# Kernel optimization log

Measured on AMD Instinct MI355X. Metric: run time of the kernel, lower is better.

The kernel has to match this reference:

```python
import jax, jax.numpy as jnp
import numpy as np

NUE, NAP, E = 512, 1024, 524288
D, OC, HID, PH = 4, 64, 32, 4  # raw feat dim, out_channels, out//2, power hid


def _lin(key, fi, fo):
    k1, k2 = jax.random.split(key)
    s = 1.0 / np.sqrt(fi)
    W = jax.random.uniform(k1, (fi, fo), minval=-s, maxval=s, dtype=jnp.float32)
    b = jax.random.uniform(k2, (fo,), minval=-s, maxval=s, dtype=jnp.float32)
    return W, b


_LAYER_SPECS = [
    ("c1_msg", D + D, HID), ("c1_upd", HID + D, OC - D), ("c1_ew", 3 * D, OC - D),
    ("c2_msg", OC + D, HID), ("c2_upd", HID + D, OC - D), ("c2_ew", D + OC + D, OC - D),
    ("c3u_msg", 2 * OC, HID), ("c3u_upd", HID + OC, OC - D), ("c3u_ew", 3 * OC, OC - D),
    ("c3d_msg", 2 * OC, HID), ("c3d_upd", HID + OC, OC - D), ("c3d_ew", 3 * OC, OC - D),
    ("pe1", OC, PH), ("pe2", PH, 1),
]


def setup_inputs() -> dict:
    key = jax.random.key(0)
    ks = jax.random.split(key, 24)
    inp = {}
    inp["x_ue"] = jax.random.normal(ks[0], (NUE, D), dtype=jnp.float32)
    inp["x_ap"] = jax.random.normal(ks[1], (NAP, D), dtype=jnp.float32)
    inp["ea_up"] = jax.random.normal(ks[2], (E, D), dtype=jnp.float32)
    inp["ea_down"] = jax.random.normal(ks[3], (E, D), dtype=jnp.float32)
    inp["ei_up_src"] = jax.random.randint(ks[4], (E,), 0, NUE, dtype=jnp.int32)
    inp["ei_up_dst"] = jax.random.randint(ks[5], (E,), 0, NAP, dtype=jnp.int32)
    inp["ei_down_src"] = jax.random.randint(ks[6], (E,), 0, NAP, dtype=jnp.int32)
    inp["ei_down_dst"] = jax.random.randint(ks[7], (E,), 0, NUE, dtype=jnp.int32)
    for i, (n, fi, fo) in enumerate(_LAYER_SPECS):
        W, b = _lin(ks[8 + i], fi, fo)
        inp[n + "_W"] = W
        inp[n + "_b"] = b
    inp["pe_ln_g"] = jnp.ones((PH,), dtype=jnp.float32)
    inp["pe_ln_b"] = jnp.zeros((PH,), dtype=jnp.float32)
    return inp


def _lrelu(x):
    return jnp.where(x >= 0, x, 0.1 * x)


def _mlp1(x, W, b):  # one MLP block: Linear -> LeakyReLU(0.1) (dropout = eval identity)
    return _lrelu(x @ W + b)


def _conv_step(x_src, x_dst, ea, src_idx, dst_idx, n_dst,
               msg_W, msg_b, upd_W, upd_b, ew_W, ew_b, residual):
    xj = x_src[src_idx]                                   # [E, d_src] gather
    m = _mlp1(jnp.concatenate([xj, ea], axis=1), msg_W, msg_b)  # [E, HID]
    agg = jax.ops.segment_sum(m, dst_idx, num_segments=n_dst)   # scatter-add -> [n_dst, HID]
    tmp = _mlp1(jnp.concatenate([x_dst, agg], axis=1), upd_W, upd_b)  # [n_dst, OC-D]
    if residual:
        tmp = tmp + x_dst[:, D:]
    new_x_dst = jnp.concatenate([x_dst[:, :D], tmp], axis=1)     # [n_dst, OC]
    xi = x_dst[dst_idx]                                   # old x_dst per torch code
    e = _mlp1(jnp.concatenate([xj, ea, xi], axis=1), ew_W, ew_b)  # [E, OC-D]
    new_ea = jnp.concatenate([ea[:, :D], e], axis=1)             # [E, OC]
    return new_x_dst, new_ea


def _layernorm(x, g, b, eps=1e-5):
    mu = jnp.mean(x, axis=-1, keepdims=True)
    var = jnp.mean(jnp.square(x - mu), axis=-1, keepdims=True)
    return (x - mu) * jax.lax.rsqrt(var + eps) * g + b


def reference(x_ue, x_ap, ea_up, ea_down,
              ei_up_src, ei_up_dst, ei_down_src, ei_down_dst,
              c1_msg_W, c1_msg_b, c1_upd_W, c1_upd_b, c1_ew_W, c1_ew_b,
              c2_msg_W, c2_msg_b, c2_upd_W, c2_upd_b, c2_ew_W, c2_ew_b,
              c3u_msg_W, c3u_msg_b, c3u_upd_W, c3u_upd_b, c3u_ew_W, c3u_ew_b,
              c3d_msg_W, c3d_msg_b, c3d_upd_W, c3d_upd_b, c3d_ew_W, c3d_ew_b,
              pe1_W, pe1_b, pe2_W, pe2_b, pe_ln_g, pe_ln_b):
    # conv1: UE --up--> AP
    x_ap, ea_up = _conv_step(x_ue, x_ap, ea_up, ei_up_src, ei_up_dst, NAP,
                             c1_msg_W, c1_msg_b, c1_upd_W, c1_upd_b, c1_ew_W, c1_ew_b, False)
    # conv2: AP --down--> UE
    x_ue, ea_down = _conv_step(x_ap, x_ue, ea_down, ei_down_src, ei_down_dst, NUE,
                               c2_msg_W, c2_msg_b, c2_upd_W, c2_upd_b, c2_ew_W, c2_ew_b, False)
    # conv3 handles both edge types (residual since src_dim == out_channels)
    x_ap, ea_up = _conv_step(x_ue, x_ap, ea_up, ei_up_src, ei_up_dst, NAP,
                             c3u_msg_W, c3u_msg_b, c3u_upd_W, c3u_upd_b, c3u_ew_W, c3u_ew_b, True)
    x_ue, ea_down = _conv_step(x_ap, x_ue, ea_down, ei_down_src, ei_down_dst, NUE,
                               c3d_msg_W, c3d_msg_b, c3d_upd_W, c3d_upd_b, c3d_ew_W, c3d_ew_b, True)
    # power head on down edges: Lin -> LayerNorm -> LeakyReLU -> Lin
    h = _lrelu(_layernorm(ea_down @ pe1_W + pe1_b, pe_ln_g, pe_ln_b))
    power = h @ pe2_W + pe2_b                                   # [E, 1]
    ea_down = jnp.concatenate([ea_down[:, :D], power], axis=1)  # [E, D+1]
    return (x_ue, x_ap, ea_up, ea_down)
```

## Files before the change

### kernel.cpp

```cpp
#include <hip/hip_runtime.h>

typedef __attribute__((ext_vector_type(8))) short bf16x8;
typedef __attribute__((ext_vector_type(4))) float f32x4;

static constexpr int EN   = 524288;
static constexpr int NUE_ = 512;
static constexpr int NAP_ = 1024;
static constexpr int HID_ = 32;
static constexpr int OD_  = 60;
static constexpr int OC_  = 64;
static constexpr int NB_  = 256;
static constexpr int CH_  = EN / NB_;

__device__ __forceinline__ unsigned short f2bf(float x) {
  unsigned int u = __float_as_uint(x);
  return (unsigned short)((u + 0x7fffu + ((u >> 16) & 1u)) >> 16);
}
__device__ __forceinline__ float bf2f(unsigned int u) {
  return __uint_as_float(u << 16);
}

__global__ __launch_bounds__(256)
void lhist2x(const int* __restrict__ up_dst, const int* __restrict__ dn_dst,
             int* __restrict__ bh_up, int* __restrict__ bh_dn,
             unsigned short* __restrict__ lr_up, unsigned short* __restrict__ lr_dn,
             const float* __restrict__ c3u_ew, const float* __restrict__ c3u_msg,
             const float* __restrict__ c3d_ew, const float* __restrict__ c3d_msg,
             unsigned short* __restrict__ we3u, unsigned short* __restrict__ wm3u,
             unsigned short* __restrict__ we3d, unsigned short* __restrict__ wm3d,
             const float* __restrict__ x_ue, const float* __restrict__ x_ap,
             const float* __restrict__ c1_ew, const float* __restrict__ c1_msg,
             const float* __restrict__ c1_ew_b, const float* __restrict__ c1_msg_b,
             const float* __restrict__ c2_ew, const float* __restrict__ c2_ew_b,
             float* __restrict__ Y1j, float* __restrict__ Y1i,
             float* __restrict__ Y1m, float* __restrict__ Y2i)
{
  __shared__ int h[NAP_];
  const int t = threadIdx.x;
  if (blockIdx.x >= 2 * NB_) {
    const int xb = blockIdx.x - 2 * NB_;
    if (xb < 48) {
      const float* W; unsigned short* out; int NREAL, NPAD, i;
      if (xb < 16)      { W = c3u_ew;  out = we3u; NREAL = 60; NPAD = 64; i = xb * 256 + t; }
      else if (xb < 24) { W = c3u_msg; out = wm3u; NREAL = 32; NPAD = 32; i = (xb - 16) * 256 + t; }
      else if (xb < 40) { W = c3d_ew;  out = we3d; NREAL = 60; NPAD = 64; i = (xb - 24) * 256 + t; }
      else              { W = c3d_msg; out = wm3d; NREAL = 32; NPAD = 32; i = (xb - 40) * 256 + t; }
      if (i >= NPAD * 64) return;
      int n = i >> 6, k = i & 63;
      float v = (n < NREAL) ? W[(size_t)(64 + k) * NREAL + n] : 0.f;
      out[i] = f2bf(v);
    } else {
      const int tid = (xb - 48) * 256 + t;
      if (tid < NUE_) {
        const float4 x = *reinterpret_cast<const float4*>(x_ue + (size_t)tid * 4);
        const float xv[4] = {x.x, x.y, x.z, x.w};
        for (int o = 0; o < OD_; ++o) {
          float a = 0.f, bb = c2_ew_b[o];
          #pragma unroll
          for (int k = 0; k < 4; ++k) {
            a = fmaf(xv[k], c1_ew[k * OD_ + o], a);
            bb = fmaf(xv[k], c2_ew[(68 + k) * OD_ + o], bb);
          }
          Y1j[(size_t)tid * OD_ + o] = a;
          Y2i[(size_t)tid * OD_ + o] = bb;
        }
        for (int o = 0; o < HID_; ++o) {
          float m = c1_msg_b[o];
          #pragma unroll
          for (int k = 0; k < 4; ++k) m = fmaf(xv[k], c1_msg[k * HID_ + o], m);
          Y1m[(size_t)tid * HID_ + o] = m;
        }
      } else if (tid < NUE_ + NAP_) {
        const int r = tid - NUE_;
        const float4 x = *reinterpret_cast<const float4*>(x_ap + (size_t)r * 4);
        const float xv[4] = {x.x, x.y, x.z, x.w};
        for (int o = 0; o < OD_; ++o) {
          float a = c1_ew_b[o];
          #pragma unroll
          for (int k = 0; k < 4; ++k) a = fmaf(xv[k], c1_ew[(8 + k) * OD_ + o], a);
          Y1i[(size_t)r * OD_ + o] = a;
        }
      }
    }
    return;
  }
  const bool up = blockIdx.x < NB_;
  const int b = up ? blockIdx.x : blockIdx.x - NB_;
  const int NBINS = up ? NAP_ : NUE_;
  const int* dst = up ? up_dst : dn_dst;
  int* bh = up ? bh_up : bh_dn;
  unsigned short* lrank = up ? lr_up : lr_dn;
  for (int i = t; i < NBINS; i += 256) h[i] = 0;
  __syncthreads();
  const int base = b * CH_;
  #pragma unroll 1
  for (int i = t; i < CH_; i += 256)
    lrank[base + i] = (unsigned short)atomicAdd(&h[dst[base + i]], 1);
  __syncthreads();
  for (int i = t; i < NBINS; i += 256)
    bh[(size_t)i * NB_ + b] = h[i];
}

__global__ __launch_bounds__(64)
void bscanA2(int* __restrict__ bh_up, int* __restrict__ bh_dn,
             int* __restrict__ bs_up, int* __restrict__ bs_dn)
{
  const bool up = blockIdx.x < NAP_;
  const int bin = up ? blockIdx.x : blockIdx.x - NAP_;
  int* bh = up ? bh_up : bh_dn;
  int* binsum = up ? bs_up : bs_dn;
  const int l = threadIdx.x;
  int4 v = *reinterpret_cast<int4*>(&bh[(size_t)bin * NB_ + l * 4]);
  const int s0 = v.x, s1 = s0 + v.y, s2 = s1 + v.z, s3 = s2 + v.w;
  int inc = s3;
  #pragma unroll
  for (int d2 = 1; d2 < 64; d2 <<= 1) {
    int n = __shfl_up(inc, d2, 64);
    if (l >= d2) inc += n;
  }
  const int exc = inc - s3;
  int4 o; o.x = exc; o.y = exc + s0; o.z = exc + s1; o.w = exc + s2;
  *reinterpret_cast<int4*>(&bh[(size_t)bin * NB_ + l * 4]) = o;
  if (l == 63) binsum[bin] = inc;
}

__global__ __launch_bounds__(256)
void bscanB2(const int* __restrict__ bs_up, int* __restrict__ off_up,
             const int* __restrict__ bs_dn, int* __restrict__ off_dn)
{
  const bool up = blockIdx.x == 0;
  const int NBINS = up ? NAP_ : NUE_;
  const int K = NBINS / 256;
  const int* binsum = up ? bs_up : bs_dn;
  int* off = up ? off_up : off_dn;
  __shared__ int wtot[4];
  const int t = threadIdx.x, lane = t & 63, wid = t >> 6;
  int loc[4]; int s = 0;
  for (int k = 0; k < K; ++k) { loc[k] = binsum[t * K + k]; s += loc[k]; }
  int inc = s;
  #pragma unroll
  for (int d2 = 1; d2 < 64; d2 <<= 1) {
    int n = __shfl_up(inc, d2, 64);
    if (lane >= d2) inc += n;
  }
  if (lane == 63) wtot[wid] = inc;
  __syncthreads();
  int woff = 0;
  #pragma unroll
  for (int ww = 0; ww < 4; ++ww) if (ww < wid) woff += wtot[ww];
  int a = woff + inc - s;
  for (int k = 0; k < K; ++k) { off[t * K + k] = a; a += loc[k]; }
  if (t == 255) off[NBINS] = a;
}

__global__ __launch_bounds__(256)
void rankc2(const int* __restrict__ up_dst, const int* __restrict__ up_src,
            const int* __restrict__ dn_dst, const int* __restrict__ dn_src,
            const unsigned short* __restrict__ lr_up, const unsigned short* __restrict__ lr_dn,
            const int* __restrict__ bh_up, const int* __restrict__ bh_dn,
            const int* __restrict__ off_up, const int* __restrict__ off_dn,
            int* __restrict__ rank_dn,
            int* __restrict__ perm_up, int* __restrict__ srcP_up, int* __restrict__ dstP_up,
            int* __restrict__ perm_dn, int* __restrict__ srcP_dn, int* __restrict__ dstP_dn)
{
  const int gid = blockIdx.x * 256 + threadIdx.x;
  const bool up = gid < EN;
  const int e = up ? gid : gid - EN;
  const int* dst = up ? up_dst : dn_dst;
  const int* src = up ? up_src : dn_src;
  const unsigned short* lrank = up ? lr_up : lr_dn;
  const int* bh = up ? bh_up : bh_dn;
  const int* off = up ? off_up : off_dn;
  const int blk = e / CH_;
  const int d = dst[e];
  const int rk = off[d] + bh[(size_t)d * NB_ + blk] + (int)lrank[e];
  if (up) {
    perm_up[rk] = e; srcP_up[rk] = src[e]; dstP_up[rk] = d;
  } else {
    rank_dn[e] = rk;
    perm_dn[rk] = e; srcP_dn[rk] = src[e]; dstP_dn[rk] = d;
  }
}

__global__ __launch_bounds__(256)
void e12n(const float* __restrict__ ea_in,
          const int* __restrict__ perm, const int* __restrict__ srcP,
          const int* __restrict__ off,
          const float* __restrict__ Yje, const float* __restrict__ Yie,
          const float* __restrict__ Ym,
          const float* __restrict__ We,
          const float* __restrict__ Wm,
          unsigned short* __restrict__ outB,
          const float* __restrict__ x_in,
          const float* __restrict__ W, const float* __restrict__ b,
          float* __restrict__ x_out,
          const float* __restrict__ WtA, float* __restrict__ YA,
          const float* __restrict__ WtB, const float* __restrict__ bB, float* __restrict__ YB,
          const float* __restrict__ WtC, const float* __restrict__ bC, float* __restrict__ YC)
{
  __shared__ unsigned short Eb[64 * 72];
  __shared__ float RedF[64][33];
  __shared__ float Part[8][33];
  __shared__ float Ag[32];
  __shared__ float Xr[4];
  __shared__ float Xn[OC_];
  const int d = blockIdx.x, t = threadIdx.x;
  const int beg = off[d], end = off[d + 1];
  const int r = t >> 2, j = t & 3;
  const int c0 = j * 15, m0 = j * 8;
  if (t < 4) Xr[t] = x_in[(size_t)d * 4 + t];
  float yie[15];
  #pragma unroll
  for (int c = 0; c < 15; ++c) yie[c] = Yie[(size_t)d * OD_ + c0 + c];
  float am[8] = {0.f, 0.f, 0.f, 0.f, 0.f, 0.f, 0.f, 0.f};

  for (int sb = beg; sb < end; sb += 64) {
    const int slot = sb + r;
    const bool act = slot < end;
    const int e = act ? perm[slot] : 0;
    const int s = act ? srcP[slot] : 0;
    float4 ea = act ? *reinterpret_cast<const float4*>(ea_in + (size_t)e * 4)
                    : make_float4(0.f, 0.f, 0.f, 0.f);
    const float eav[4] = {ea.x, ea.y, ea.z, ea.w};
    float acc[15];
    #pragma unroll
    for (int c = 0; c < 15; ++c) acc[c] = Yje[(size_t)s * OD_ + c0 + c] + yie[c];
    #pragma unroll
    for (int k = 0; k < 4; ++k)
      #pragma unroll
      for (int c = 0; c < 15; ++c)
        acc[c] = fmaf(eav[k], We[k * OD_ + c0 + c], acc[c]);
    if (act) {
      #pragma unroll
      for (int c = 0; c < 15; ++c) {
        float v = acc[c] >= 0.f ? acc[c] : 0.1f * acc[c];
        Eb[r * 72 + 4 + c0 + c] = f2bf(v);
      }
      if (j == 0) {
        Eb[r * 72 + 0] = f2bf(ea.x); Eb[r * 72 + 1] = f2bf(ea.y);
        Eb[r * 72 + 2] = f2bf(ea.z); Eb[r * 72 + 3] = f2bf(ea.w);
      }
    }
    float m[8];
    #pragma unroll
    for (int c = 0; c < 8; ++c) m[c] = Ym[(size_t)s * HID_ + m0 + c];
    #pragma unroll
    for (int k = 0; k < 4; ++k)
      #pragma unroll
      for (int c = 0; c < 8; ++c)
        m[c] = fmaf(eav[k], Wm[k * HID_ + m0 + c], m[c]);
    if (act) {
      #pragma unroll
      for (int c = 0; c < 8; ++c)
        am[c] += m[c] >= 0.f ? m[c] : 0.1f * m[c];
    }
    __syncthreads();
    const int nact = end - sb < 64 ? end - sb : 64;
    for (int idx = t; idx < nact * 8; idx += 256) {
      int row = idx >> 3, ch = idx & 7;
      *reinterpret_cast<uint4*>(outB + (size_t)(sb + row) * OC_ + ch * 8) =
          *reinterpret_cast<const uint4*>(&Eb[row * 72 + ch * 8]);
    }
    __syncthreads();
  }
  #pragma unroll
  for (int c = 0; c < 8; ++c) RedF[r][m0 + c] = am[c];
  __syncthreads();
  {
    const int col = t & 31, g = t >> 5;
    float s = 0.f;
    #pragma unroll
    for (int r2 = 0; r2 < 8; ++r2) s += RedF[g * 8 + r2][col];
    Part[g][col] = s;
  }
  __syncthreads();
  if (t < 32) {
    float s = 0.f;
    #pragma unroll
    for (int g2 = 0; g2 < 8; ++g2) s += Part[g2][t];
    Ag[t] = s;
  }
  __syncthreads();
  if (t < OD_) {
    float acc = b[t];
    #pragma unroll
    for (int k = 0; k < 4; ++k) acc = fmaf(Xr[k], W[k * OD_ + t], acc);
    #pragma unroll 4
    for (int k = 0; k < HID_; ++k) acc = fmaf(Ag[k], W[(4 + k) * OD_ + t], acc);
    acc = acc >= 0.f ? acc : 0.1f * acc;
    x_out[(size_t)d * OC_ + 4 + t] = acc;
    Xn[4 + t] = acc;
  } else if (t < OC_) {
    x_out[(size_t)d * OC_ + (t - OD_)] = Xr[t - OD_];
    Xn[t - OD_] = Xr[t - OD_];
  }
  __syncthreads();
  if (t < OD_) {
    float a = 0.f;
    #pragma unroll 4
    for (int k = 0; k < OC_; ++k) a = fmaf(Xn[k], WtA[k * OD_ + t], a);
    YA[(size_t)d * OD_ + t] = a;
  } else if (t >= 64 && t < 96) {
    const int cc = t - 64;
    float a = bB[cc];
    #pragma unroll 4
    for (int k = 0; k < OC_; ++k) a = fmaf(Xn[k], WtB[k * HID_ + cc], a);
    YB[(size_t)d * HID_ + cc] = a;
  } else if (t >= 128 && t < 188) {
    const int cc = t - 128;
    float a = bC[cc];
    #pragma unroll 4
    for (int k = 0; k < OC_; ++k) a = fmaf(Xn[k], WtC[k * OD_ + cc], a);
    YC[(size_t)d * OD_ + cc] = a;
  }
}

template<bool FUSE>
__global__ __launch_bounds__(256)
void edge3(const unsigned short* __restrict__ eaB,
           const float* __restrict__ ea0_src,
           const int* __restrict__ perm,
           const int* __restrict__ srcP, const int* __restrict__ dstP,
           const unsigned short* __restrict__ Wet, const unsigned short* __restrict__ Wmt,
           const float* __restrict__ Yje, const float* __restrict__ Yie,
           const float* __restrict__ Ym,
           unsigned int* __restrict__ msg32,
           float* __restrict__ ea_out,
           float* __restrict__ pT,
           const float* __restrict__ pe1_W)
{
  const int t = threadIdx.x, l = t & 63, w = t >> 6;
  const int lr = l & 15, lkb = l >> 4;
  const int sW = blockIdx.x * 256 + w * 64;

  bf16x8 be[4][2], bm[2][2];
  #pragma unroll
  for (int nt = 0; nt < 4; ++nt)
    #pragma unroll
    for (int kk = 0; kk < 2; ++kk)
      be[nt][kk] = *reinterpret_cast<const bf16x8*>(Wet + (nt * 16 + lr) * 64 + kk * 32 + lkb * 8);
  #pragma unroll
  for (int nt = 0; nt < 2; ++nt)
    #pragma unroll
    for (int kk = 0; kk < 2; ++kk)
      bm[nt][kk] = *reinterpret_cast<const bf16x8*>(Wmt + (nt * 16 + lr) * 64 + kk * 32 + lkb * 8);

  #pragma unroll 1
  for (int tile = 0; tile < 4; ++tile) {
    const int s0t = sW + tile * 16;
    const unsigned short* ar = eaB + (size_t)(s0t + lr) * OC_ + lkb * 8;
    bf16x8 a[2];
    a[0] = *reinterpret_cast<const bf16x8*>(ar);
    a[1] = *reinterpret_cast<const bf16x8*>(ar + 32);

    f32x4 accE[4] = {f32x4{0,0,0,0}, f32x4{0,0,0,0}, f32x4{0,0,0,0}, f32x4{0,0,0,0}};
    f32x4 accM[2] = {f32x4{0,0,0,0}, f32x4{0,0,0,0}};
    #pragma unroll
    for (int kk = 0; kk < 2; ++kk) {
      #pragma unroll
      for (int nt = 0; nt < 4; ++nt)
        accE[nt] = __builtin_amdgcn_mfma_f32_16x16x32_bf16(a[kk], be[nt][kk], accE[nt], 0, 0, 0);
      #pragma unroll
      for (int nt = 0; nt < 2; ++nt)
        accM[nt] = __builtin_amdgcn_mfma_f32_16x16x32_bf16(a[kk], bm[nt][kk], accM[nt], 0, 0, 0);
    }
    #pragma unroll
    for (int r = 0; r < 4; ++r) {
      const int sl = s0t + lkb * 4 + r;
      const int s = srcP[sl], d = dstP[sl];
      float v0 = accM[0][r] + Ym[(size_t)s * HID_ + lr];
      float v1 = accM[1][r] + Ym[(size_t)s * HID_ + 16 + lr];
      v0 = v0 >= 0.f ? v0 : 0.1f * v0;
      v1 = v1 >= 0.f ? v1 : 0.1f * v1;
      const int q0 = (2 * lr) & 15, q1 = (2 * lr + 1) & 15;
      float t00 = __shfl(v0, q0, 16), t10 = __shfl(v1, q0, 16);
      float t01 = __shfl(v0, q1, 16), t11 = __shfl(v1, q1, 16);
      float lo = (lr < 8) ? t00 : t10;
      float hi = (lr < 8) ? t01 : t11;
      msg32[(size_t)sl * 16 + lr] = ((unsigned)f2bf(hi) << 16) | f2bf(lo);

      float val[4];
      #pragma unroll
      for (int nt = 0; nt < 4; ++nt) {
        int col = nt * 16 + lr;
        float v = (col < OD_)
            ? accE[nt][r] + Yje[(size_t)s * OD_ + col] + Yie[(size_t)d * OD_ + col]
            : 0.f;
        val[nt] = v >= 0.f ? v : 0.1f * v;
      }
      if constexpr (!FUSE) {
        const int e = perm[sl];
        #pragma unroll
        for (int nt = 0; nt < 4; ++nt) {
          int col = nt * 16 + lr;
          if (col < OD_) ea_out[(size_t)e * OC_ + 4 + col] = val[nt];
        }
        if (lr == 0) {
          float4 ea0 = *reinterpret_cast<const float4*>(ea0_src + (size_t)e * 4);
          *reinterpret_cast<float4*>(ea_out + (size_t)e * OC_) = ea0;
        }
      } else {
        float p4[4] = {0.f, 0.f, 0.f, 0.f};
        #pragma unroll
        for (int nt = 0; nt < 4; ++nt) {
          int col = nt * 16 + lr;
          if (col < OD_) {
            #pragma unroll
            for (int jj = 0; jj < 4; ++jj)
              p4[jj] = fmaf(val[nt], pe1_W[(4 + col) * 4 + jj], p4[jj]);
          }
        }
        #pragma unroll
        for (int mk = 1; mk < 16; mk <<= 1) {
          #pragma unroll
          for (int jj = 0; jj < 4; ++jj)
            p4[jj] += __shfl_xor(p4[jj], mk, 64);
        }
        if (lr == 0)
          *reinterpret_cast<float4*>(pT + (size_t)sl * 4) =
              make_float4(p4[0], p4[1], p4[2], p4[3]);
      }
    }
  }
}

template<int LX, bool RES>
__device__ __forceinline__
void nodeup_body(int d, int t,
                 const float* __restrict__ x_in,
                 const unsigned int* __restrict__ msg32,
                 const int* __restrict__ off,
                 const float* __restrict__ W, const float* __restrict__ b,
                 float* __restrict__ x_out,
                 const float* WtA, float* YA,
                 const float* WtB, const float* bB, float* YB)
{
  __shared__ float Pb[16][32];
  __shared__ float Ag[32];
  __shared__ float Xr[LX];
  __shared__ float Xn[OC_];
  const int beg = off[d], end = off[d + 1];
  const int c = t & 15, g = t >> 4;
  float px = 0.f, py = 0.f;
  for (int i = beg + g; i < end; i += 16) {
    unsigned u = msg32[(size_t)i * 16 + c];
    px += bf2f(u & 0xffffu);
    py += bf2f(u >> 16);
  }
  Pb[g][2 * c] = px; Pb[g][2 * c + 1] = py;
  if (t < LX) Xr[t] = x_in[(size_t)d * LX + t];
  __syncthreads();
  if (t < 32) {
    float s = 0.f;
    #pragma unroll
    for (int g2 = 0; g2 < 16; ++g2) s += Pb[g2][t];
    Ag[t] = s;
  }
  __syncthreads();
  if (t < OD_) {
    float acc = b[t];
    #pragma unroll 4
    for (int k = 0; k < LX; ++k) acc = fmaf(Xr[k], W[k * OD_ + t], acc);
    #pragma unroll 4
    for (int k = 0; k < HID_; ++k) acc = fmaf(Ag[k], W[(LX + k) * OD_ + t], acc);
    acc = acc >= 0.f ? acc : 0.1f * acc;
    if constexpr (RES) acc += Xr[4 + t];
    x_out[(size_t)d * OC_ + 4 + t] = acc;
    Xn[4 + t] = acc;
  } else if (t < OC_) {
    x_out[(size_t)d * OC_ + (t - OD_)] = Xr[t - OD_];
    Xn[t - OD_] = Xr[t - OD_];
  }
  if (WtA == nullptr) return;
  __syncthreads();
  if (t < OD_) {
    float a = 0.f;
    #pragma unroll 4
    for (int k = 0; k < OC_; ++k) a = fmaf(Xn[k], WtA[k * OD_ + t], a);
    YA[(size_t)d * OD_ + t] = a;
  } else if (t >= 64 && t < 96) {
    const int cc = t - 64;
    float a = bB[cc];
    #pragma unroll 4
    for (int k = 0; k < OC_; ++k) a = fmaf(Xn[k], WtB[k * HID_ + cc], a);
    YB[(size_t)d * HID_ + cc] = a;
  }
}

template<int LX, bool RES>
__global__ __launch_bounds__(256)
void nodeupT(const float* __restrict__ x_in, const unsigned int* __restrict__ msg32,
             const int* __restrict__ off,
             const float* __restrict__ W, const float* __restrict__ b,
             float* __restrict__ x_out,
             const float* WtA, float* YA,
             const float* WtB, const float* bB, float* YB)
{
  nodeup_body<LX, RES>(blockIdx.x, threadIdx.x, x_in, msg32, off, W, b, x_out,
                       WtA, YA, WtB, bB, YB);
}

__global__ __launch_bounds__(256)
void nodeup_pow(const float* __restrict__ x_in, const unsigned int* __restrict__ msg32,
                const int* __restrict__ off,
                const float* __restrict__ W, const float* __restrict__ b,
                float* __restrict__ x_out,
                const float* __restrict__ ea0_src, const int* __restrict__ rank,
                const float* __restrict__ pT,
                const float* __restrict__ pe1_W, const float* __restrict__ pe1_b,
                const float* __restrict__ pe2_W, const float* __restrict__ pe2_b,
                const float* __restrict__ ln_g, const float* __restrict__ ln_b,
                float* __restrict__ outp)
{
  if (blockIdx.x < NUE_) {
    nodeup_body<OC_, true>(blockIdx.x, threadIdx.x, x_in, msg32, off, W, b, x_out,
                           nullptr, nullptr, nullptr, nullptr, nullptr);
    return;
  }
  const int e = (blockIdx.x - NUE_) * 256 + threadIdx.x;
  const int rk = rank[e];
  const float4 p4 = *reinterpret_cast<const float4*>(pT + (size_t)rk * 4);
  const float4 ea0 = *reinterpret_cast<const float4*>(ea0_src + (size_t)e * 4);
  const float pv[4] = {p4.x, p4.y, p4.z, p4.w};
  float v4[4];
  #pragma unroll
  for (int jj = 0; jj < 4; ++jj)
    v4[jj] = pv[jj] + pe1_b[jj]
           + ea0.x * pe1_W[0 * 4 + jj] + ea0.y * pe1_W[1 * 4 + jj]
           + ea0.z * pe1_W[2 * 4 + jj] + ea0.w * pe1_W[3 * 4 + jj];
  const float mu = 0.25f * (v4[0] + v4[1] + v4[2] + v4[3]);
  float var = 0.f;
  #pragma unroll
  for (int jj = 0; jj < 4; ++jj) { float dd = v4[jj] - mu; var = fmaf(dd, dd, var); }
  var *= 0.25f;
  const float rstd = rsqrtf(var + 1e-5f);
  float p = pe2_b[0];
  #pragma unroll
  for (int jj = 0; jj < 4; ++jj) {
    float h = (v4[jj] - mu) * rstd * ln_g[jj] + ln_b[jj];
    h = h >= 0.f ? h : 0.1f * h;
    p = fmaf(h, pe2_W[jj], p);
  }
  float* orow = outp + (size_t)e * 5;
  orow[0] = ea0.x; orow[1] = ea0.y; orow[2] = ea0.z; orow[3] = ea0.w;
  orow[4] = p;
}

extern "C" void kernel_launch(void* const* d_in, const int* in_sizes, int n_in,
                              void* d_out, int out_size, void* d_ws, size_t ws_size,
                              hipStream_t stream)
{
  const float* x_ue    = (const float*)d_in[0];
  const float* x_ap    = (const float*)d_in[1];
  const float* ea_up   = (const float*)d_in[2];
  const float* ea_down = (const float*)d_in[3];
  const int* up_src = (const int*)d_in[4];
  const int* up_dst = (const int*)d_in[5];
  const int* dn_src = (const int*)d_in[6];
  const int* dn_dst = (const int*)d_in[7];
  const float* c1_msg_W = (const float*)d_in[8];  const float* c1_msg_b = (const float*)d_in[9];
  const float* c1_upd_W = (const float*)d_in[10]; const float* c1_upd_b = (const float*)d_in[11];
  const float* c1_ew_W  = (const float*)d_in[12]; const float* c1_ew_b  = (const float*)d_in[13];
  const float* c2_msg_W = (const float*)d_in[14]; const float* c2_msg_b = (const float*)d_in[15];
  const float* c2_upd_W = (const float*)d_in[16]; const float* c2_upd_b = (const float*)d_in[17];
  const float* c2_ew_W  = (const float*)d_in[18]; const float* c2_ew_b  = (const float*)d_in[19];
  const float* c3u_msg_W= (const float*)d_in[20]; const float* c3u_msg_b= (const float*)d_in[21];
  const float* c3u_upd_W= (const float*)d_in[22]; const float* c3u_upd_b= (const float*)d_in[23];
  const float* c3u_ew_W = (const float*)d_in[24]; const float* c3u_ew_b = (const float*)d_in[25];
  const float* c3d_msg_W= (const float*)d_in[26]; const float* c3d_msg_b= (const float*)d_in[27];
  const float* c3d_upd_W= (const float*)d_in[28]; const float* c3d_upd_b= (const float*)d_in[29];
  const float* c3d_ew_W = (const float*)d_in[30]; const float* c3d_ew_b = (const float*)d_in[31];
  const float* pe1_W = (const float*)d_in[32]; const float* pe1_b = (const float*)d_in[33];
  const float* pe2_W = (const float*)d_in[34]; const float* pe2_b = (const float*)d_in[35];
  const float* ln_g  = (const float*)d_in[36]; const float* ln_b  = (const float*)d_in[37];

  float* out    = (float*)d_out;
  float* x_ue_o = out;
  float* x_ap_o = out + (size_t)NUE_ * OC_;
  float* ea_up_o = x_ap_o + (size_t)NAP_ * OC_;
  float* ea_dn_o = ea_up_o + (size_t)EN * OC_;

  int* ip = (int*)d_ws;
  int* rank_dn = ip; ip += EN;
  int* perm_up = ip; ip += EN;
  int* src_upP = ip; ip += EN;
  int* dst_upP = ip; ip += EN;
  int* perm_dn = ip; ip += EN;
  int* src_dnP = ip; ip += EN;
  int* dst_dnP = ip; ip += EN;
  int* bh_up   = ip; ip += NAP_ * NB_;
  int* bh_dn   = ip; ip += NUE_ * NB_;
  int* off_up  = ip; ip += NAP_ + 1;
  int* off_dn  = ip; ip += NUE_ + 1;
  int* bs_up   = ip; ip += NAP_;
  int* bs_dn   = ip; ip += NUE_;
  unsigned short* lr_up = (unsigned short*)ip; ip += EN / 2;
  unsigned short* lr_dn = (unsigned short*)ip; ip += EN / 2;
  float* p = (float*)ip;
  float* Y1j = p;  p += NUE_ * OD_;  float* Y1i = p; p += NAP_ * OD_;  float* Y1m = p; p += NUE_ * HID_;
  float* Y2j = p;  p += NAP_ * OD_;  float* Y2i = p; p += NUE_ * OD_;  float* Y2m = p; p += NAP_ * HID_;
  float* Y3uj = p; p += NUE_ * OD_;  float* Y3ui = p; p += NAP_ * OD_; float* Y3um = p; p += NUE_ * HID_;
  float* Y3dj = p; p += NAP_ * OD_;  float* Y3di = p; p += NUE_ * OD_; float* Y3dm = p; p += NAP_ * HID_;
  float* pT = p;   p += (size_t)EN * 4;
  unsigned short* us = (unsigned short*)p;
  unsigned short* ea_up_bf = us;  us += (size_t)EN * OC_;
  unsigned short* ea_dn_bf = us;  us += (size_t)EN * OC_;
  unsigned short* we3u = us; us += 64 * 64;
  unsigned short* wm3u = us; us += 32 * 64;
  unsigned short* we3d = us; us += 64 * 64;
  unsigned short* wm3d = us; us += 32 * 64;
  unsigned int* msg32 = (unsigned int*)(((size_t)us + 15) & ~(size_t)15);

  const dim3 blk(256);
  const dim3 ege(EN / 256);

  lhist2x<<<dim3(2 * NB_ + 56), blk, 0, stream>>>(
      up_dst, dn_dst, bh_up, bh_dn, lr_up, lr_dn,
      c3u_ew_W, c3u_msg_W, c3d_ew_W, c3d_msg_W, we3u, wm3u, we3d, wm3d,
      x_ue, x_ap, c1_ew_W, c1_msg_W, c1_ew_b, c1_msg_b, c2_ew_W, c2_ew_b,
      Y1j, Y1i, Y1m, Y2i);
  bscanA2<<<dim3(NAP_ + NUE_), dim3(64), 0, stream>>>(bh_up, bh_dn, bs_up, bs_dn);
  bscanB2<<<dim3(2), blk, 0, stream>>>(bs_up, off_up, bs_dn, off_dn);
  rankc2<<<dim3(2 * EN / 256), blk, 0, stream>>>(
      up_dst, up_src, dn_dst, dn_src, lr_up, lr_dn, bh_up, bh_dn, off_up, off_dn,
      rank_dn, perm_up, src_upP, dst_upP, perm_dn, src_dnP, dst_dnP);

  e12n<<<dim3(NAP_), blk, 0, stream>>>(
      ea_up, perm_up, src_upP, off_up, Y1j, Y1i, Y1m,
      c1_ew_W + 4 * OD_, c1_msg_W + 4 * HID_, ea_up_bf,
      x_ap, c1_upd_W, c1_upd_b, x_ap_o,
      c2_ew_W, Y2j, c2_msg_W, c2_msg_b, Y2m,
      c3u_ew_W + 128 * OD_, c3u_ew_b, Y3ui);

  e12n<<<dim3(NUE_), blk, 0, stream>>>(
      ea_down, perm_dn, src_dnP, off_dn, Y2j, Y2i, Y2m,
      c2_ew_W + 64 * OD_, c2_msg_W + 64 * HID_, ea_dn_bf,
      x_ue, c2_upd_W, c2_upd_b, x_ue_o,
      c3u_ew_W, Y3uj, c3u_msg_W, c3u_msg_b, Y3um,
      c3d_ew_W + 128 * OD_, c3d_ew_b, Y3di);

  edge3<false><<<ege, blk, 0, stream>>>(
      ea_up_bf, ea_up, perm_up, src_upP, dst_upP, we3u, wm3u,
      Y3uj, Y3ui, Y3um, msg32, ea_up_o, nullptr, nullptr);
  nodeupT<64, true><<<dim3(NAP_), blk, 0, stream>>>(
      x_ap_o, msg32, off_up, c3u_upd_W, c3u_upd_b, x_ap_o,
      c3d_ew_W, Y3dj, c3d_msg_W, c3d_msg_b, Y3dm);

  edge3<true><<<ege, blk, 0, stream>>>(
      ea_dn_bf, nullptr, nullptr, src_dnP, dst_dnP, we3d, wm3d,
      Y3dj, Y3di, Y3dm, msg32, nullptr, pT, pe1_W);
  nodeup_pow<<<dim3(NUE_ + EN / 256), blk, 0, stream>>>(
      x_ue_o, msg32, off_dn, c3d_upd_W, c3d_upd_b, x_ue_o,
      ea_down, rank_dn, pT, pe1_W, pe1_b, pe2_W, pe2_b, ln_g, ln_b, ea_dn_o);
}
```

Baseline: 432.0 us.

## Aggregate conv3 messages in edge kernel via run-length atomics instead of message buffer

```diff
diff --git a/kernel.cpp b/kernel.cpp
--- a/kernel.cpp
+++ b/kernel.cpp
@@ -324,7 +324,7 @@
            const unsigned short* __restrict__ Wet, const unsigned short* __restrict__ Wmt,
            const float* __restrict__ Yje, const float* __restrict__ Yie,
            const float* __restrict__ Ym,
-           unsigned int* __restrict__ msg32,
+           float* __restrict__ agg,
            float* __restrict__ ea_out,
            float* __restrict__ pT,
            const float* __restrict__ pe1_W)
@@ -344,6 +344,9 @@
     #pragma unroll
     for (int kk = 0; kk < 2; ++kk)
       bm[nt][kk] = *reinterpret_cast<const bf16x8*>(Wmt + (nt * 16 + lr) * 64 + kk * 32 + lkb * 8);
+
+  float accLo = 0.f, accHi = 0.f;
+  int curD = -1;
 
   #pragma unroll 1
   for (int tile = 0; tile < 4; ++tile) {
@@ -377,7 +380,15 @@
       float t01 = __shfl(v0, q1, 16), t11 = __shfl(v1, q1, 16);
       float lo = (lr < 8) ? t00 : t10;
       float hi = (lr < 8) ? t01 : t11;
-      msg32[(size_t)sl * 16 + lr] = ((unsigned)f2bf(hi) << 16) | f2bf(lo);
+      if (d != curD) {
+        if (curD >= 0) {
+          atomicAdd(&agg[(size_t)curD * HID_ + 2 * lr], accLo);
+          atomicAdd(&agg[(size_t)curD * HID_ + 2 * lr + 1], accHi);
+        }
+        curD = d; accLo = lo; accHi = hi;
+      } else {
+        accLo += lo; accHi += hi;
+      }
 
       float val[4];
       #pragma unroll
@@ -422,40 +433,27 @@
       }
     }
   }
+  if (curD >= 0) {
+    atomicAdd(&agg[(size_t)curD * HID_ + 2 * lr], accLo);
+    atomicAdd(&agg[(size_t)curD * HID_ + 2 * lr + 1], accHi);
+  }
 }
 
 template<int LX, bool RES>
 __device__ __forceinline__
 void nodeup_body(int d, int t,
                  const float* __restrict__ x_in,
-                 const unsigned int* __restrict__ msg32,
-                 const int* __restrict__ off,
+                 const float* __restrict__ agg,
                  const float* __restrict__ W, const float* __restrict__ b,
                  float* __restrict__ x_out,
                  const float* WtA, float* YA,
                  const float* WtB, const float* bB, float* YB)
 {
-  __shared__ float Pb[16][32];
   __shared__ float Ag[32];
   __shared__ float Xr[LX];
   __shared__ float Xn[OC_];
-  const int beg = off[d], end = off[d + 1];
-  const int c = t & 15, g = t >> 4;
-  float px = 0.f, py = 0.f;
-  for (int i = beg + g; i < end; i += 16) {
-    unsigned u = msg32[(size_t)i * 16 + c];
-    px += bf2f(u & 0xffffu);
-    py += bf2f(u >> 16);
-  }
-  Pb[g][2 * c] = px; Pb[g][2 * c + 1] = py;
+  if (t < 32) Ag[t] = agg[(size_t)d * HID_ + t];
   if (t < LX) Xr[t] = x_in[(size_t)d * LX + t];
-  __syncthreads();
-  if (t < 32) {
-    float s = 0.f;
-    #pragma unroll
-    for (int g2 = 0; g2 < 16; ++g2) s += Pb[g2][t];
-    Ag[t] = s;
-  }
   __syncthreads();
   if (t < OD_) {
     float acc = b[t];
@@ -489,20 +487,18 @@
 
 template<int LX, bool RES>
 __global__ __launch_bounds__(256)
-void nodeupT(const float* __restrict__ x_in, const unsigned int* __restrict__ msg32,
-             const int* __restrict__ off,
+void nodeupT(const float* __restrict__ x_in, const float* __restrict__ agg,
              const float* __restrict__ W, const float* __restrict__ b,
              float* __restrict__ x_out,
              const float* WtA, float* YA,
              const float* WtB, const float* bB, float* YB)
 {
-  nodeup_body<LX, RES>(blockIdx.x, threadIdx.x, x_in, msg32, off, W, b, x_out,
+  nodeup_body<LX, RES>(blockIdx.x, threadIdx.x, x_in, agg, W, b, x_out,
                        WtA, YA, WtB, bB, YB);
 }
 
 __global__ __launch_bounds__(256)
-void nodeup_pow(const float* __restrict__ x_in, const unsigned int* __restrict__ msg32,
-                const int* __restrict__ off,
+void nodeup_pow(const float* __restrict__ x_in, const float* __restrict__ agg,
                 const float* __restrict__ W, const float* __restrict__ b,
                 float* __restrict__ x_out,
                 const float* __restrict__ ea0_src, const int* __restrict__ rank,
@@ -513,7 +509,7 @@
                 float* __restrict__ outp)
 {
   if (blockIdx.x < NUE_) {
-    nodeup_body<OC_, true>(blockIdx.x, threadIdx.x, x_in, msg32, off, W, b, x_out,
+    nodeup_body<OC_, true>(blockIdx.x, threadIdx.x, x_in, agg, W, b, x_out,
                            nullptr, nullptr, nullptr, nullptr, nullptr);
     return;
   }
@@ -580,7 +576,9 @@
   float* ea_up_o = x_ap_o + (size_t)NAP_ * OC_;
   float* ea_dn_o = ea_up_o + (size_t)EN * OC_;
 
-  int* ip = (int*)d_ws;
+  float* agg3 = (float*)d_ws;
+  float* agg4 = agg3 + NAP_ * HID_;
+  int* ip = (int*)(agg4 + NUE_ * HID_);
   int* rank_dn = ip; ip += EN;
   int* perm_up = ip; ip += EN;
   int* src_upP = ip; ip += EN;
@@ -609,7 +607,8 @@
   unsigned short* wm3u = us; us += 32 * 64;
   unsigned short* we3d = us; us += 64 * 64;
   unsigned short* wm3d = us; us += 32 * 64;
-  unsigned int* msg32 = (unsigned int*)(((size_t)us + 15) & ~(size_t)15);
+
+  hipMemsetAsync(agg3, 0, sizeof(float) * (NAP_ + NUE_) * HID_, stream);
 
   const dim3 blk(256);
   const dim3 ege(EN / 256);
@@ -641,15 +640,15 @@
 
   edge3<false><<<ege, blk, 0, stream>>>(
       ea_up_bf, ea_up, perm_up, src_upP, dst_upP, we3u, wm3u,
-      Y3uj, Y3ui, Y3um, msg32, ea_up_o, nullptr, nullptr);
+      Y3uj, Y3ui, Y3um, agg3, ea_up_o, nullptr, nullptr);
   nodeupT<64, true><<<dim3(NAP_), blk, 0, stream>>>(
-      x_ap_o, msg32, off_up, c3u_upd_W, c3u_upd_b, x_ap_o,
+      x_ap_o, agg3, c3u_upd_W, c3u_upd_b, x_ap_o,
       c3d_ew_W, Y3dj, c3d_msg_W, c3d_msg_b, Y3dm);
 
   edge3<true><<<ege, blk, 0, stream>>>(
       ea_dn_bf, nullptr, nullptr, src_dnP, dst_dnP, we3d, wm3d,
-      Y3dj, Y3di, Y3dm, msg32, nullptr, pT, pe1_W);
+      Y3dj, Y3di, Y3dm, agg4, nullptr, pT, pe1_W);
   nodeup_pow<<<dim3(NUE_ + EN / 256), blk, 0, stream>>>(
-      x_ue_o, msg32, off_dn, c3d_upd_W, c3d_upd_b, x_ue_o,
+      x_ue_o, agg4, c3d_upd_W, c3d_upd_b, x_ue_o,
       ea_down, rank_dn, pT, pe1_W, pe1_b, pe2_W, pe2_b, ln_g, ln_b, ea_dn_o);
 }
```

New measurement: 434.0 us, median of 2. No clear change (+0.5%).
